# Kernel tuning notes

Hardware: AMD Instinct MI355X
Metric: run time of the kernel (lower is better)

## Reference

```python
import jax, jax.numpy as jnp
import numpy as np

B, S, D = 4, 2048, 1024
H, HD = 16, 64
WINDOW = 256


def setup_inputs() -> dict:
    key = jax.random.key(0)
    ks = jax.random.split(key, 5)
    scale = 1.0 / np.sqrt(D)
    return {
        "hidden_states": jax.random.normal(ks[0], (B, S, D), dtype=jnp.float32),
        "Wq": jax.random.normal(ks[1], (D, D), dtype=jnp.float32) * scale,
        "Wk": jax.random.normal(ks[2], (D, D), dtype=jnp.float32) * scale,
        "Wv": jax.random.normal(ks[3], (D, D), dtype=jnp.float32) * scale,
        "Wo": jax.random.normal(ks[4], (D, D), dtype=jnp.float32) * scale,
        "bo": jnp.zeros((D,), dtype=jnp.float32),
    }


def reference(hidden_states, Wq, Wk, Wv, Wo, bo):
    # q/k/v projections (no bias), torch Linear: x @ W.T
    q = hidden_states @ Wq.T  # [B,S,D]
    k = hidden_states @ Wk.T
    v = hidden_states @ Wv.T

    def split_heads(t):  # [B,S,D] -> [B,H,S,HD]
        return t.reshape(B, S, H, HD).transpose(0, 2, 1, 3)

    q, k, v = split_heads(q), split_heads(k), split_heads(v)

    # NOTE: original code does NOT scale by 1/sqrt(head_dim)
    scores = jnp.einsum("bhqd,bhkd->bhqk", q.astype(jnp.float32), k.astype(jnp.float32))

    # local causal band mask: keep j <= i and i - j < WINDOW
    i = jnp.arange(S)[:, None]
    j = jnp.arange(S)[None, :]
    band = (j <= i) & (i - j < WINDOW)  # [S,S] bool
    mask_value = jnp.finfo(scores.dtype).min
    scores = jnp.where(band[None, None, :, :], scores, mask_value)

    attn = jax.nn.softmax(scores, axis=-1).astype(v.dtype)
    ctx = jnp.einsum("bhqk,bhkd->bhqd", attn, v)  # [B,H,S,HD]

    # merge heads -> [B,S,D]
    ctx = ctx.transpose(0, 2, 1, 3).reshape(B, S, D)
    out = ctx @ Wo.T + bo
    return out
```

## Files before the change

### kernel.cpp

```cpp
#include <hip/hip_runtime.h>
#include <hip/hip_bf16.h>
#include <cstdint>
#include <cstddef>

#define S_LEN   2048
#define BATCH   4
#define NHEAD   16
#define HDIM    64
#define DMODEL  1024
#define WIN     256
#define PQ      72

typedef __bf16 bf16x8 __attribute__((ext_vector_type(8)));
typedef float f32x4 __attribute__((ext_vector_type(4)));
typedef unsigned short u16x4 __attribute__((ext_vector_type(4)));
typedef unsigned short u16x8 __attribute__((ext_vector_type(8)));

__device__ __forceinline__ unsigned short f2bf(float x) {
  union { float f; unsigned u; } c; c.f = x;
  unsigned r = (c.u + 0x7fffu + ((c.u >> 16) & 1u)) >> 16;
  return (unsigned short)r;
}

__device__ __forceinline__ void gld_lds16(const void* g, void* l) {
  __builtin_amdgcn_global_load_lds(
      (__attribute__((address_space(1))) void*)g,
      (__attribute__((address_space(3))) void*)l, 16, 0, 0);
}

__global__ __launch_bounds__(256) void convert_kernel(
    const float* __restrict__ s0, const float* __restrict__ s1,
    const float* __restrict__ s2, const float* __restrict__ s3,
    const float* __restrict__ s4,
    unsigned short* __restrict__ d0, unsigned short* __restrict__ d1,
    unsigned short* __restrict__ d2, unsigned short* __restrict__ d3,
    unsigned short* __restrict__ d4) {
  const int z = blockIdx.y;
  const float* s; unsigned short* d; long n;
  if      (z == 0) { s = s0; d = d0; n = (long)8192 * 1024; }
  else if (z == 1) { s = s1; d = d1; n = (long)1024 * 1024; }
  else if (z == 2) { s = s2; d = d2; n = (long)1024 * 1024; }
  else if (z == 3) { s = s3; d = d3; n = (long)1024 * 1024; }
  else             { s = s4; d = d4; n = (long)1024 * 1024; }
  const long base = ((long)blockIdx.x * 256 + threadIdx.x) * 16;
  if (base >= n) return;
#pragma unroll
  for (int i = 0; i < 4; ++i) {
    const float4 f = *(const float4*)(s + base + i * 4);
    u16x4 ov;
    ov.x = f2bf(f.x); ov.y = f2bf(f.y); ov.z = f2bf(f.z); ov.w = f2bf(f.w);
    *(u16x4*)(d + base + i * 4) = ov;
  }
}

template <int MODE>
__device__ __forceinline__ void gemm_bt_core(
    const unsigned short* __restrict__ A, const unsigned short* __restrict__ B,
    void* __restrict__ C, const float* __restrict__ bias,
    int M, int N, int K,
    unsigned short* __restrict__ lsA, unsigned short* __restrict__ lsB) {
  const int m0 = blockIdx.x * 128;
  const int n0 = blockIdx.y * 128;
  const int tid  = threadIdx.x;
  const int wave = tid >> 6, lane = tid & 63;
  const int quad = lane >> 4, l16 = lane & 15;
  const int wm = wave >> 1, wn = wave & 1;

  f32x4 acc[4][4];
#pragma unroll
  for (int i = 0; i < 4; ++i)
#pragma unroll
    for (int j = 0; j < 4; ++j) acc[i][j] = f32x4{0.f, 0.f, 0.f, 0.f};

  const int trow   = tid >> 3;
  const int tchunk = tid & 7;
  const int swz_w  = (trow >> 1) & 7;
  const int scol   = ((tchunk ^ swz_w) << 3);
  const int swz_r  = (l16 >> 1) & 7;

  for (int k0 = 0; k0 < K; k0 += 64) {
    __syncthreads();
#pragma unroll
    for (int c = 0; c < 4; ++c) {
      const int row  = trow + 32 * c;
      const int flat = row * 64 + tchunk * 8;
      gld_lds16(A + (size_t)(m0 + row) * K + k0 + scol, lsA + flat);
      gld_lds16(B + (size_t)(n0 + row) * K + k0 + scol, lsB + flat);
    }
    __syncthreads();

#pragma unroll
    for (int s2 = 0; s2 < 2; ++s2) {
      bf16x8 af[4], bfr[4];
#pragma unroll
      for (int mi = 0; mi < 4; ++mi)
        af[mi] = *(const bf16x8*)(lsA + (wm * 64 + mi * 16 + l16) * 64 +
                                  (((s2 * 4 + quad) ^ swz_r) << 3));
#pragma unroll
      for (int ni = 0; ni < 4; ++ni)
        bfr[ni] = *(const bf16x8*)(lsB + (wn * 64 + ni * 16 + l16) * 64 +
                                   (((s2 * 4 + quad) ^ swz_r) << 3));
#pragma unroll
      for (int mi = 0; mi < 4; ++mi)
#pragma unroll
        for (int ni = 0; ni < 4; ++ni)
          acc[mi][ni] = __builtin_amdgcn_mfma_f32_16x16x32_bf16(
              af[mi], bfr[ni], acc[mi][ni], 0, 0, 0);
    }
  }

#pragma unroll
  for (int mi = 0; mi < 4; ++mi) {
    if (MODE == 2) {
      const int mB = m0 + wm * 64 + mi * 16 + quad * 4;
      const int bq = mB >> 11, s = mB & 2047;
#pragma unroll
      for (int ni = 0; ni < 4; ++ni) {
        const int n = n0 + wn * 64 + ni * 16 + l16;
        u16x4 w;
        w[0] = f2bf(acc[mi][ni][0]); w[1] = f2bf(acc[mi][ni][1]);
        w[2] = f2bf(acc[mi][ni][2]); w[3] = f2bf(acc[mi][ni][3]);
        *(u16x4*)((unsigned short*)C +
                  (((size_t)((bq << 4) | (n >> 6)) * 64 + (n & 63)) << 11) + s) = w;
      }
    } else {
#pragma unroll
      for (int r = 0; r < 4; ++r) {
        const int m = m0 + wm * 64 + mi * 16 + quad * 4 + r;
#pragma unroll
        for (int ni = 0; ni < 4; ++ni) {
          const int n = n0 + wn * 64 + ni * 16 + l16;
          const float vv = acc[mi][ni][r];
          if (MODE == 0) {
            ((unsigned short*)C)[(size_t)m * N + n] = f2bf(vv);
          } else {
            ((float*)C)[(size_t)m * N + n] = vv + bias[n];
          }
        }
      }
    }
  }
}

__global__ __launch_bounds__(256) void gemm_qkv_kernel(
    const unsigned short* __restrict__ A,
    const unsigned short* __restrict__ B0, const unsigned short* __restrict__ B1,
    const unsigned short* __restrict__ B2,
    unsigned short* __restrict__ C0, unsigned short* __restrict__ C1,
    unsigned short* __restrict__ Cv, int M, int N, int K) {
  __shared__ unsigned short lsA[128 * 64];
  __shared__ unsigned short lsB[128 * 64];
  if (blockIdx.z == 2) {
    gemm_bt_core<2>(A, B2, Cv, nullptr, M, N, K, lsA, lsB);
  } else {
    const unsigned short* B = blockIdx.z == 0 ? B0 : B1;
    unsigned short*       C = blockIdx.z == 0 ? C0 : C1;
    gemm_bt_core<0>(A, B, C, nullptr, M, N, K, lsA, lsB);
  }
}

__global__ __launch_bounds__(256) void gemm_out_kernel(
    const unsigned short* __restrict__ A, const unsigned short* __restrict__ B,
    float* __restrict__ C, const float* __restrict__ bias, int M, int N, int K) {
  __shared__ unsigned short lsA[128 * 64];
  __shared__ unsigned short lsB[128 * 64];
  gemm_bt_core<1>(A, B, C, bias, M, N, K, lsA, lsB);
}

__global__ __launch_bounds__(256) void attn_kernel(
    const unsigned short* __restrict__ q, const unsigned short* __restrict__ k,
    const unsigned short* __restrict__ vt, unsigned short* __restrict__ ctx) {
  const int bh = blockIdx.y;
  const int b = bh >> 4, h = bh & 15;
  const int i0 = blockIdx.x * 128;
  const int tid  = threadIdx.x;
  const int wave = tid >> 6, lane = tid & 63;
  const int quad = lane >> 4, l16 = lane & 15;

  __shared__ unsigned short lsQ[128 * PQ];
  __shared__ unsigned short lsK[64 * PQ];
  __shared__ unsigned short lsVp[64 * PQ];

  {
    const int r = tid >> 1, cb = (tid & 1) * 32;
    const unsigned short* src =
        q + ((size_t)(b * S_LEN + i0 + r) * DMODEL + h * HDIM + cb);
    *(u16x8*)(lsQ + r * PQ + cb)      = *(const u16x8*)src;
    *(u16x8*)(lsQ + r * PQ + cb + 8)  = *(const u16x8*)(src + 8);
    *(u16x8*)(lsQ + r * PQ + cb + 16) = *(const u16x8*)(src + 16);
    *(u16x8*)(lsQ + r * PQ + cb + 24) = *(const u16x8*)(src + 24);
  }
  __syncthreads();

  bf16x8 aq[2][2];
#pragma unroll
  for (int t = 0; t < 2; ++t)
#pragma unroll
    for (int s2 = 0; s2 < 2; ++s2)
      aq[t][s2] = *(const bf16x8*)(lsQ + (wave * 32 + t * 16 + l16) * PQ +
                                   s2 * 32 + quad * 8);

  float l_lane[2] = {0.f, 0.f};
  f32x4 o[2][4];
#pragma unroll
  for (int t = 0; t < 2; ++t)
#pragma unroll
    for (int nd = 0; nd < 4; ++nd) o[t][nd] = f32x4{0.f, 0.f, 0.f, 0.f};

  const int jb0 = (i0 >= WIN) ? ((i0 - WIN + 1) >> 6) : 0;
  const int jb1 = (i0 + 127) >> 6;
  const int jbi = i0 >> 6;

  for (int jb = jb0; jb <= jb1; ++jb) {
    const int j0 = jb * 64;
    const bool needMask = !(jb == jbi - 1 || jb == jbi - 2);
    __syncthreads();
    {
      const int r = tid >> 2, cb = (tid & 3) * 16;
      const unsigned short* ks =
          k + ((size_t)(b * S_LEN + j0 + r) * DMODEL + h * HDIM + cb);
      *(u16x8*)(lsK + r * PQ + cb)     = *(const u16x8*)ks;
      *(u16x8*)(lsK + r * PQ + cb + 8) = *(const u16x8*)(ks + 8);
      const unsigned short* vs =
          vt + ((size_t)(bh * HDIM + r) * S_LEN + j0 + cb);
      const u16x8 va = *(const u16x8*)vs;
      const u16x8 vb = *(const u16x8*)(vs + 8);
      const int jhi = cb >> 4;
      const int base = (jhi >> 1) * 32 + (jhi & 1) * 4;
      u16x4 w0, w1, w2, w3;
      w0[0]=va[0];  w0[1]=va[1];  w0[2]=va[2];  w0[3]=va[3];
      w1[0]=va[4];  w1[1]=va[5];  w1[2]=va[6];  w1[3]=va[7];
      w2[0]=vb[0];  w2[1]=vb[1];  w2[2]=vb[2];  w2[3]=vb[3];
      w3[0]=vb[4];  w3[1]=vb[5];  w3[2]=vb[6];  w3[3]=vb[7];
      *(u16x4*)(lsVp + r * PQ + base)      = w0;
      *(u16x4*)(lsVp + r * PQ + base + 8)  = w1;
      *(u16x4*)(lsVp + r * PQ + base + 16) = w2;
      *(u16x4*)(lsVp + r * PQ + base + 24) = w3;
    }
    __syncthreads();

    f32x4 st[2][4];
#pragma unroll
    for (int t = 0; t < 2; ++t)
#pragma unroll
      for (int ni = 0; ni < 4; ++ni) st[t][ni] = f32x4{0.f, 0.f, 0.f, 0.f};
#pragma unroll
    for (int s2 = 0; s2 < 2; ++s2) {
      bf16x8 bk[4];
#pragma unroll
      for (int ni = 0; ni < 4; ++ni)
        bk[ni] = *(const bf16x8*)(lsK + (ni * 16 + l16) * PQ + s2 * 32 + quad * 8);
#pragma unroll
      for (int t = 0; t < 2; ++t)
#pragma unroll
        for (int ni = 0; ni < 4; ++ni)
          st[t][ni] = __builtin_amdgcn_mfma_f32_16x16x32_bf16(
              bk[ni], aq[t][s2], st[t][ni], 0, 0, 0);
    }

    bf16x8 ap[2][2];
#pragma unroll
    for (int t = 0; t < 2; ++t) {
      const int iq = i0 + wave * 32 + t * 16 + l16;
      if (needMask) {
#pragma unroll
        for (int ni = 0; ni < 4; ++ni)
#pragma unroll
          for (int r = 0; r < 4; ++r) {
            const int j = j0 + ni * 16 + quad * 4 + r;
            const bool ok = (j <= iq) && (iq - j < WIN);
            const float p = ok ? __expf(fminf(st[t][ni][r], 80.f)) : 0.f;
            st[t][ni][r] = p;
            l_lane[t] += p;
          }
      } else {
#pragma unroll
        for (int ni = 0; ni < 4; ++ni)
#pragma unroll
          for (int r = 0; r < 4; ++r) {
            const float p = __expf(fminf(st[t][ni][r], 80.f));
            st[t][ni][r] = p;
            l_lane[t] += p;
          }
      }
#pragma unroll
      for (int s2 = 0; s2 < 2; ++s2) {
        bf16x8 a;
#pragma unroll
        for (int r = 0; r < 4; ++r) {
          union { unsigned short u; __bf16 h; } c0, c1;
          c0.u = f2bf(st[t][2 * s2][r]);
          c1.u = f2bf(st[t][2 * s2 + 1][r]);
          a[r]     = c0.h;
          a[4 + r] = c1.h;
        }
        ap[t][s2] = a;
      }
    }

#pragma unroll
    for (int s2 = 0; s2 < 2; ++s2) {
      bf16x8 bv[4];
#pragma unroll
      for (int nd = 0; nd < 4; ++nd)
        bv[nd] = *(const bf16x8*)(lsVp + (nd * 16 + l16) * PQ + s2 * 32 + quad * 8);
#pragma unroll
      for (int t = 0; t < 2; ++t)
#pragma unroll
        for (int nd = 0; nd < 4; ++nd)
          o[t][nd] = __builtin_amdgcn_mfma_f32_16x16x32_bf16(
              ap[t][s2], bv[nd], o[t][nd], 0, 0, 0);
    }
  }

#pragma unroll
  for (int t = 0; t < 2; ++t) {
    float l = l_lane[t];
    l += __shfl_xor(l, 16, 64);
    l += __shfl_xor(l, 32, 64);
    const float invl = 1.f / l;
#pragma unroll
    for (int r = 0; r < 4; ++r) {
      const float inv = __shfl(invl, quad * 4 + r, 64);
      const int i = i0 + wave * 32 + t * 16 + quad * 4 + r;
#pragma unroll
      for (int nd = 0; nd < 4; ++nd)
        ctx[(size_t)(b * S_LEN + i) * DMODEL + h * HDIM + nd * 16 + l16] =
            f2bf(o[t][nd][r] * inv);
    }
  }
}

extern "C" void kernel_launch(void* const* d_in, const int* in_sizes, int n_in,
                              void* d_out, int out_size, void* d_ws, size_t ws_size,
                              hipStream_t stream) {
  const float* hs = (const float*)d_in[0];
  const float* Wq = (const float*)d_in[1];
  const float* Wk = (const float*)d_in[2];
  const float* Wv = (const float*)d_in[3];
  const float* Wo = (const float*)d_in[4];
  const float* bo = (const float*)d_in[5];
  float* out = (float*)d_out;

  const size_t MD = (size_t)8192 * 1024;
  const size_t DD = (size_t)1024 * 1024;
  unsigned short* hsb  = (unsigned short*)d_ws;
  unsigned short* wqb  = hsb + MD;
  unsigned short* wkb  = wqb + DD;
  unsigned short* wvb  = wkb + DD;
  unsigned short* wob  = wvb + DD;
  unsigned short* qb   = wob + DD;
  unsigned short* kb   = qb + MD;
  unsigned short* vtb  = kb + MD;
  unsigned short* ctxb = vtb + MD;

  convert_kernel<<<dim3(2048, 5), 256, 0, stream>>>(hs, Wq, Wk, Wv, Wo,
                                                    hsb, wqb, wkb, wvb, wob);
  gemm_qkv_kernel<<<dim3(64, 8, 3), 256, 0, stream>>>(hsb, wqb, wkb, wvb,
                                                      qb, kb, vtb, 8192, 1024, 1024);
  attn_kernel<<<dim3(16, 64), 256, 0, stream>>>(qb, kb, vtb, ctxb);
  gemm_out_kernel<<<dim3(64, 8), 256, 0, stream>>>(ctxb, wob, out, bo,
                                                   8192, 1024, 1024);
}
```

Before: 221.4 us.

## Prefetch next K/V tile into registers and raise wave priority around MFMA

The attention kernel now loads the next K and V tile from global memory into registers while the current tile is being computed, then writes it to LDS at the start of the next iteration. This hides global load latency behind the QK and PV matrix multiplies. It also wraps the MFMA blocks in s_setprio raises, and folds the two-sided band mask into a single unsigned compare. The cost is extra live registers for the prefetched data, which could lower occupancy.

```diff
diff --git a/kernel.cpp b/kernel.cpp
--- a/kernel.cpp
+++ b/kernel.cpp
@@ -190,6 +190,28 @@
     *(u16x8*)(lsQ + r * PQ + cb + 16) = *(const u16x8*)(src + 16);
     *(u16x8*)(lsQ + r * PQ + cb + 24) = *(const u16x8*)(src + 24);
   }
+
+  const int rr = tid >> 2, cb = (tid & 3) * 16;
+  const int jhi  = cb >> 4;
+  const int vbase = (jhi >> 1) * 32 + (jhi & 1) * 4;
+
+  const int jb0 = (i0 >= WIN) ? ((i0 - WIN + 1) >> 6) : 0;
+  const int jb1 = (i0 + 127) >> 6;
+  const int jbi = i0 >> 6;
+
+  u16x8 pk0, pk1, pv0, pv1;
+  {
+    const int j0 = jb0 * 64;
+    const unsigned short* ks =
+        k + ((size_t)(b * S_LEN + j0 + rr) * DMODEL + h * HDIM + cb);
+    pk0 = *(const u16x8*)ks;
+    pk1 = *(const u16x8*)(ks + 8);
+    const unsigned short* vs =
+        vt + ((size_t)(bh * HDIM + rr) * S_LEN + j0 + cb);
+    pv0 = *(const u16x8*)vs;
+    pv1 = *(const u16x8*)(vs + 8);
+  }
+
   __syncthreads();
 
   bf16x8 aq[2][2];
@@ -206,44 +228,44 @@
   for (int t = 0; t < 2; ++t)
 #pragma unroll
     for (int nd = 0; nd < 4; ++nd) o[t][nd] = f32x4{0.f, 0.f, 0.f, 0.f};
-
-  const int jb0 = (i0 >= WIN) ? ((i0 - WIN + 1) >> 6) : 0;
-  const int jb1 = (i0 + 127) >> 6;
-  const int jbi = i0 >> 6;
 
   for (int jb = jb0; jb <= jb1; ++jb) {
     const int j0 = jb * 64;
     const bool needMask = !(jb == jbi - 1 || jb == jbi - 2);
     __syncthreads();
     {
-      const int r = tid >> 2, cb = (tid & 3) * 16;
+      *(u16x8*)(lsK + rr * PQ + cb)     = pk0;
+      *(u16x8*)(lsK + rr * PQ + cb + 8) = pk1;
+      u16x4 w0, w1, w2, w3;
+      w0[0]=pv0[0]; w0[1]=pv0[1]; w0[2]=pv0[2]; w0[3]=pv0[3];
+      w1[0]=pv0[4]; w1[1]=pv0[5]; w1[2]=pv0[6]; w1[3]=pv0[7];
+      w2[0]=pv1[0]; w2[1]=pv1[1]; w2[2]=pv1[2]; w2[3]=pv1[3];
+      w3[0]=pv1[4]; w3[1]=pv1[5]; w3[2]=pv1[6]; w3[3]=pv1[7];
+      *(u16x4*)(lsVp + rr * PQ + vbase)      = w0;
+      *(u16x4*)(lsVp + rr * PQ + vbase + 8)  = w1;
+      *(u16x4*)(lsVp + rr * PQ + vbase + 16) = w2;
+      *(u16x4*)(lsVp + rr * PQ + vbase + 24) = w3;
+    }
+    __syncthreads();
+
+    if (jb < jb1) {
+      const int jn = j0 + 64;
       const unsigned short* ks =
-          k + ((size_t)(b * S_LEN + j0 + r) * DMODEL + h * HDIM + cb);
-      *(u16x8*)(lsK + r * PQ + cb)     = *(const u16x8*)ks;
-      *(u16x8*)(lsK + r * PQ + cb + 8) = *(const u16x8*)(ks + 8);
+          k + ((size_t)(b * S_LEN + jn + rr) * DMODEL + h * HDIM + cb);
+      pk0 = *(const u16x8*)ks;
+      pk1 = *(const u16x8*)(ks + 8);
       const unsigned short* vs =
-          vt + ((size_t)(bh * HDIM + r) * S_LEN + j0 + cb);
-      const u16x8 va = *(const u16x8*)vs;
-      const u16x8 vb = *(const u16x8*)(vs + 8);
-      const int jhi = cb >> 4;
-      const int base = (jhi >> 1) * 32 + (jhi & 1) * 4;
-      u16x4 w0, w1, w2, w3;
-      w0[0]=va[0];  w0[1]=va[1];  w0[2]=va[2];  w0[3]=va[3];
-      w1[0]=va[4];  w1[1]=va[5];  w1[2]=va[6];  w1[3]=va[7];
-      w2[0]=vb[0];  w2[1]=vb[1];  w2[2]=vb[2];  w2[3]=vb[3];
-      w3[0]=vb[4];  w3[1]=vb[5];  w3[2]=vb[6];  w3[3]=vb[7];
-      *(u16x4*)(lsVp + r * PQ + base)      = w0;
-      *(u16x4*)(lsVp + r * PQ + base + 8)  = w1;
-      *(u16x4*)(lsVp + r * PQ + base + 16) = w2;
-      *(u16x4*)(lsVp + r * PQ + base + 24) = w3;
-    }
-    __syncthreads();
+          vt + ((size_t)(bh * HDIM + rr) * S_LEN + jn + cb);
+      pv0 = *(const u16x8*)vs;
+      pv1 = *(const u16x8*)(vs + 8);
+    }
 
     f32x4 st[2][4];
 #pragma unroll
     for (int t = 0; t < 2; ++t)
 #pragma unroll
       for (int ni = 0; ni < 4; ++ni) st[t][ni] = f32x4{0.f, 0.f, 0.f, 0.f};
+    __builtin_amdgcn_s_setprio(1);
 #pragma unroll
     for (int s2 = 0; s2 < 2; ++s2) {
       bf16x8 bk[4];
@@ -257,6 +279,7 @@
           st[t][ni] = __builtin_amdgcn_mfma_f32_16x16x32_bf16(
               bk[ni], aq[t][s2], st[t][ni], 0, 0, 0);
     }
+    __builtin_amdgcn_s_setprio(0);
 
     bf16x8 ap[2][2];
 #pragma unroll
@@ -268,7 +291,7 @@
 #pragma unroll
           for (int r = 0; r < 4; ++r) {
             const int j = j0 + ni * 16 + quad * 4 + r;
-            const bool ok = (j <= iq) && (iq - j < WIN);
+            const bool ok = ((unsigned)(iq - j) < (unsigned)WIN);
             const float p = ok ? __expf(fminf(st[t][ni][r], 80.f)) : 0.f;
             st[t][ni][r] = p;
             l_lane[t] += p;
@@ -298,6 +321,7 @@
       }
     }
 
+    __builtin_amdgcn_s_setprio(1);
 #pragma unroll
     for (int s2 = 0; s2 < 2; ++s2) {
       bf16x8 bv[4];
@@ -311,6 +335,7 @@
           o[t][nd] = __builtin_amdgcn_mfma_f32_16x16x32_bf16(
               ap[t][s2], bv[nd], o[t][nd], 0, 0, 0);
     }
+    __builtin_amdgcn_s_setprio(0);
   }
 
 #pragma unroll
```

Measured after the change: 212.8 us. 1.04x faster.
